# Optimization experiments

Hardware: AMD Instinct MI355X
Metric: run time of the kernel (lower is better)

The kernel has to match this reference:

```python
import jax, jax.numpy as jnp
import numpy as np

B, C, D = 8192, 10000, 128
CLAMP_MIN, CLAMP_MAX = 1e-12, 1e12


def setup_inputs() -> dict:
    key = jax.random.key(0)
    k1, k2, k3 = jax.random.split(key, 3)
    x = jax.random.normal(k1, (B, D), dtype=jnp.float32)
    labels = jax.random.randint(k2, (B,), 0, C, dtype=jnp.int64)
    centers = jax.random.normal(k3, (C, D), dtype=jnp.float32)
    lr = jnp.array([0.1], dtype=jnp.float32)
    return {"x": x, "labels": labels, "centers": centers, "lr": lr}


def reference(x, labels, centers, lr):
    b, d = x.shape
    c = centers.shape[0]
    # --- vectorized center update (replaces double python loop) ---
    # A_j = count_j * centers[j] - sum_{i: labels_i==j} x_i ; delta_j = A_j / (1 + count_j)
    counts = jax.ops.segment_sum(jnp.ones((b,), dtype=x.dtype), labels, num_segments=c)  # [C]
    sum_x = jax.ops.segment_sum(x, labels, num_segments=c)                               # [C, D]
    delta = (counts[:, None] * centers - sum_x) / (1.0 + counts[:, None])
    centers = centers - lr * delta
    # --- squared euclidean distance matrix [B, C] ---
    distmat = (
        jnp.sum(x * x, axis=1, keepdims=True)
        + jnp.sum(centers * centers, axis=1)[None, :]
        - 2.0 * (x @ centers.T)
    )
    git = 1.0 / (1.0 + distmat)
    # gather own-class entries (replaces per-sample mask loop)
    lab = labels[:, None]
    center_vals = jnp.take_along_axis(distmat, lab, axis=1)[:, 0]          # [B]
    git_vals = jnp.sum(git, axis=1) - jnp.take_along_axis(git, lab, axis=1)[:, 0]
    center_loss = jnp.mean(jnp.clip(center_vals, CLAMP_MIN, CLAMP_MAX))
    git_loss = jnp.mean(jnp.clip(git_vals, CLAMP_MIN, CLAMP_MAX))
    return (center_loss, git_loss)
```

## Files before the change

### kernel.cpp

```cpp
#include <hip/hip_runtime.h>
#include <hip/hip_bf16.h>
#include <hip/hip_fp8.h>

#define B_ 8192
#define C_ 10000
#define D_ 128
#define CPAD 10112
#define NPADC 112
#define NT_TOT 158
#define NSTRIP 16
#define STRIPW 10
#define UPD_BLOCKS 2528
#define CVAL_BLOCKS 2048

typedef float f32x4 __attribute__((ext_vector_type(4)));
typedef int   i32x8 __attribute__((ext_vector_type(8)));

typedef const __attribute__((address_space(1))) uint32_t gu32;
typedef __attribute__((address_space(3))) uint32_t lu32;


__global__ void zero_ws(float4* __restrict__ ws, float* __restrict__ out) {
    int idx = blockIdx.x * 256 + threadIdx.x;
    if (idx < 324608) ws[idx] = float4{0.f, 0.f, 0.f, 0.f};
    if (idx == 0) { out[0] = 0.f; out[1] = 0.f; }
}

__global__ void scatter_prep(const float* __restrict__ x, const int* __restrict__ labels,
                             float* __restrict__ counts, float* __restrict__ sumx,
                             float* __restrict__ xnorm, unsigned char* __restrict__ xb8) {
    int tid = threadIdx.x;
    int w = tid >> 6, lane = tid & 63;
    int i = blockIdx.x * 4 + w;
    int l = labels[i];
    float2 v = *(const float2*)&x[i * D_ + lane * 2];
    atomicAdd(&sumx[l * D_ + lane * 2], v.x);
    atomicAdd(&sumx[l * D_ + lane * 2 + 1], v.y);
    if (lane == 0) atomicAdd(&counts[l], 1.0f);
    __hip_fp8_e4m3 a(v.x), b(v.y);
    unsigned short pk = (unsigned short)a.__x | ((unsigned short)b.__x << 8);
    *(unsigned short*)&xb8[i * D_ + lane * 2] = pk;
    float s = v.x * v.x + v.y * v.y;
    #pragma unroll
    for (int m = 1; m < 64; m <<= 1) s += __shfl_xor(s, m);
    if (lane == 0) xnorm[i] = s;
}

__global__ void upd_cvals(const float* __restrict__ centers, const float* __restrict__ counts,
                          const float* __restrict__ sumx, float* __restrict__ cnorm,
                          unsigned char* __restrict__ cb8, const float* __restrict__ lr,
                          const float* __restrict__ x, const int* __restrict__ labels,
                          float* __restrict__ cent_val) {
    int tid = threadIdx.x;
    int w = tid >> 6, lane = tid & 63;
    int bid = blockIdx.x;
    float lrv = lr[0];

    if (bid < UPD_BLOCKS) {
        int c = bid * 4 + w;
        if (c >= C_) {
            *(unsigned short*)&cb8[c * D_ + lane * 2] = 0;
            if (lane == 0) cnorm[c] = 0.0f;
            return;
        }
        float cnt = counts[c];
        float2 cv = *(const float2*)&centers[c * D_ + lane * 2];
        float2 sx = *(const float2*)&sumx[c * D_ + lane * 2];
        float inv = 1.0f / (1.0f + cnt);
        float nx = cv.x - lrv * (cnt * cv.x - sx.x) * inv;
        float ny = cv.y - lrv * (cnt * cv.y - sx.y) * inv;
        __hip_fp8_e4m3 a(nx), b(ny);
        unsigned short pk = (unsigned short)a.__x | ((unsigned short)b.__x << 8);
        *(unsigned short*)&cb8[c * D_ + lane * 2] = pk;
        float s = nx * nx + ny * ny;
        #pragma unroll
        for (int m = 1; m < 64; m <<= 1) s += __shfl_xor(s, m);
        if (lane == 0) cnorm[c] = s;
    } else {
        int i = (bid - UPD_BLOCKS) * 4 + w;
        int l = labels[i];
        float cnt = counts[l];
        float inv = 1.0f / (1.0f + cnt);
        float2 a  = *(const float2*)&x[i * D_ + lane * 2];
        float2 cv = *(const float2*)&centers[l * D_ + lane * 2];
        float2 sx = *(const float2*)&sumx[l * D_ + lane * 2];
        float nx = cv.x - lrv * (cnt * cv.x - sx.x) * inv;
        float ny = cv.y - lrv * (cnt * cv.y - sx.y) * inv;
        float dx = a.x - nx, dy = a.y - ny;
        float s = dx * dx + dy * dy;
        #pragma unroll
        for (int m = 1; m < 64; m <<= 1) s += __shfl_xor(s, m);
        if (lane == 0) cent_val[i] = s;
    }
}

__global__ void __launch_bounds__(256, 2)
gemm_git(const unsigned char* __restrict__ xb8, const unsigned char* __restrict__ cb8,
         const float* __restrict__ xnorm, const float* __restrict__ cnorm,
         float* __restrict__ git_row) {
    __shared__ char ldsB[3][8192];
    __shared__ float cnLDS[STRIPW * 64];

    int tid = threadIdx.x;
    int w = tid >> 6, lane = tid & 63;
    int lr_ = lane & 15, lg = lane >> 4;
    int bm = blockIdx.x;
    int strip = blockIdx.y;
    int row0 = bm * 256 + w * 64;
    int bn0 = strip * STRIPW;
    int nt = (strip == NSTRIP - 1) ? (NT_TOT - bn0) : STRIPW;

    i32x8 af[4];
    #pragma unroll
    for (int f = 0; f < 4; f++) {
        const uint4* pa = (const uint4*)(xb8 + (size_t)(row0 + f * 16 + lr_) * 128 + lg * 32);
        uint4 u0 = pa[0], u1 = pa[1];
        asm volatile("" : "+v"(u0.x), "+v"(u0.y), "+v"(u0.z), "+v"(u0.w),
                          "+v"(u1.x), "+v"(u1.y), "+v"(u1.z), "+v"(u1.w));
        af[f] = i32x8{(int)u0.x, (int)u0.y, (int)u0.z, (int)u0.w,
                      (int)u1.x, (int)u1.y, (int)u1.z, (int)u1.w};
    }

    float xn1[4][4];
    #pragma unroll
    for (int fm = 0; fm < 4; fm++)
        #pragma unroll
        for (int r = 0; r < 4; r++) {
            float v = 1.0f + xnorm[row0 + fm * 16 + lg * 4 + r];
            asm volatile("" : "+v"(v));
            xn1[fm][r] = v;
        }

    float gitsum[4][4] = {};

    const char* gB = (const char*)cb8;
    int sr0 = tid >> 3,          sc0 = (tid & 7) ^ (sr0 & 7);
    int sr1 = (tid + 256) >> 3,  sc1 = ((tid + 256) & 7) ^ (sr1 & 7);
    size_t goff0 = (size_t)sr0 * 128 + sc0 * 16;
    size_t goff1 = (size_t)sr1 * 128 + sc1 * 16;

    auto stage = [&](int t, int buf) {
        const char* base = gB + (size_t)(bn0 + t) * 64 * 128;
        __builtin_amdgcn_global_load_lds((gu32*)(base + goff0),
                                         (lu32*)&ldsB[buf][tid * 16], 16, 0, 0);
        __builtin_amdgcn_global_load_lds((gu32*)(base + goff1),
                                         (lu32*)&ldsB[buf][4096 + tid * 16], 16, 0, 0);
    };

    for (int i = tid; i < nt * 64; i += 256) cnLDS[i] = cnorm[bn0 * 64 + i];
    stage(0, 0);
    if (nt > 1) stage(1, 1);
    __syncthreads();

    for (int t = 0; t < nt; ++t) {
        int bc = t % 3;
        if (t + 2 < nt) stage(t + 2, (t + 2) % 3);

        if (t + 2 < nt)      asm volatile("s_waitcnt vmcnt(4)" ::: "memory");
        else if (t + 1 < nt) asm volatile("s_waitcnt vmcnt(2)" ::: "memory");
        else                 asm volatile("s_waitcnt vmcnt(0)" ::: "memory");
        __builtin_amdgcn_sched_barrier(0);
        __builtin_amdgcn_s_barrier();
        __builtin_amdgcn_sched_barrier(0);

        float cn[4];
        #pragma unroll
        for (int fn = 0; fn < 4; fn++) cn[fn] = cnLDS[t * 64 + fn * 16 + lr_];

        i32x8 bfk[4];
        int r7 = lr_ & 7;
        #pragma unroll
        for (int fn = 0; fn < 4; fn++) {
            const char* rowp = &ldsB[bc][(fn * 16 + lr_) * 128];
            uint4 q0 = *(const uint4*)(rowp + (((lg * 2)     ^ r7) * 16));
            uint4 q1 = *(const uint4*)(rowp + (((lg * 2 + 1) ^ r7) * 16));
            bfk[fn] = i32x8{(int)q0.x, (int)q0.y, (int)q0.z, (int)q0.w,
                            (int)q1.x, (int)q1.y, (int)q1.z, (int)q1.w};
        }

        f32x4 acc[4][4] = {};
        __builtin_amdgcn_s_setprio(1);
        #pragma unroll
        for (int fm = 0; fm < 4; fm++)
            #pragma unroll
            for (int fn = 0; fn < 4; fn++)
                acc[fm][fn] = __builtin_amdgcn_mfma_scale_f32_16x16x128_f8f6f4(
                    af[fm], bfk[fn], acc[fm][fn],
                    0, 0,
                    0, 0x7F,
                    0, 0x7F);
        __builtin_amdgcn_s_setprio(0);

        #pragma unroll
        for (int fm = 0; fm < 4; fm++)
            #pragma unroll
            for (int r = 0; r < 4; r++) {
                float base = xn1[fm][r];
                #pragma unroll
                for (int fp = 0; fp < 4; fp += 2) {
                    float u = base + cn[fp]     - 2.0f * acc[fm][fp][r];
                    float v = base + cn[fp + 1] - 2.0f * acc[fm][fp + 1][r];
                    gitsum[fm][r] += (u + v) * __builtin_amdgcn_rcpf(u * v);
                }
            }

        __builtin_amdgcn_sched_barrier(0);
        __builtin_amdgcn_s_barrier();
        __builtin_amdgcn_sched_barrier(0);
    }

    #pragma unroll
    for (int fm = 0; fm < 4; fm++)
        #pragma unroll
        for (int r = 0; r < 4; r++) {
            float s = gitsum[fm][r];
            s += __shfl_xor(s, 1); s += __shfl_xor(s, 2);
            s += __shfl_xor(s, 4); s += __shfl_xor(s, 8);
            if (lr_ == 0) atomicAdd(&git_row[row0 + fm * 16 + lg * 4 + r], s);
        }
}

__global__ void final_reduce(const float* __restrict__ cent_val, const float* __restrict__ git_row,
                             const float* __restrict__ xnorm, float* __restrict__ out) {
    int tid = threadIdx.x;
    int i = blockIdx.x * 256 + tid;
    float c = cent_val[i];
    float cl = fminf(fmaxf(c, 1e-12f), 1e12f);
    float g = git_row[i] - 1.0f / (1.0f + c) - (float)NPADC / (1.0f + xnorm[i]);
    float gl = fminf(fmaxf(g, 1e-12f), 1e12f);
    #pragma unroll
    for (int m = 1; m < 64; m <<= 1) { cl += __shfl_xor(cl, m); gl += __shfl_xor(gl, m); }
    __shared__ float scl[4], sgl[4];
    if ((tid & 63) == 0) { scl[tid >> 6] = cl; sgl[tid >> 6] = gl; }
    __syncthreads();
    if (tid == 0) {
        float a = scl[0] + scl[1] + scl[2] + scl[3];
        float b = sgl[0] + sgl[1] + sgl[2] + sgl[3];
        atomicAdd(&out[0], a / (float)B_);
        atomicAdd(&out[1], b / (float)B_);
    }
}

extern "C" void kernel_launch(void* const* d_in, const int* in_sizes, int n_in,
                              void* d_out, int out_size, void* d_ws, size_t ws_size,
                              hipStream_t stream) {
    const float* x       = (const float*)d_in[0];
    const int*   labels  = (const int*)d_in[1];
    const float* centers = (const float*)d_in[2];
    const float* lr      = (const float*)d_in[3];

    float* ws       = (float*)d_ws;
    float* counts   = ws;
    float* sumx     = ws + 10240;
    float* git_row  = ws + 1290240;
    float* xnorm    = ws + 1298432;
    float* cent_val = ws + 1306624;
    float* cnorm    = ws + 1314816;
    unsigned char* xb8 = (unsigned char*)d_ws + 5300224;
    unsigned char* cb8 = (unsigned char*)d_ws + 7397376;
    float* out = (float*)d_out;

    zero_ws<<<1268, 256, 0, stream>>>((float4*)d_ws, out);
    scatter_prep<<<B_ / 4, 256, 0, stream>>>(x, labels, counts, sumx, xnorm, xb8);
    upd_cvals<<<UPD_BLOCKS + CVAL_BLOCKS, 256, 0, stream>>>(centers, counts, sumx, cnorm, cb8, lr,
                                                            x, labels, cent_val);
    gemm_git<<<dim3(32, NSTRIP), 256, 0, stream>>>(xb8, cb8, xnorm, cnorm, git_row);
    final_reduce<<<32, 256, 0, stream>>>(cent_val, git_row, xnorm, out);
}
```

Before: 50.29 us.

## Stage two center tiles per pipeline step and drop the trailing barrier

Each LDS stage of the FP8 GEMM now holds two 64-column center tiles instead of one, so the triple-buffered loop runs half as many iterations. The prefetch of stage s+2 is issued right after the per-iteration barrier, into the buffer freed by iteration s-1. That lets the end-of-iteration barrier go, leaving one barrier per two tiles instead of two per tile. The cost is double the LDS per block (48KB) and a longer gap between each wait and its consumer, which could limit occupancy or exposed latency.

```diff
diff --git a/kernel.cpp b/kernel.cpp
--- a/kernel.cpp
+++ b/kernel.cpp
@@ -98,7 +98,7 @@
 gemm_git(const unsigned char* __restrict__ xb8, const unsigned char* __restrict__ cb8,
          const float* __restrict__ xnorm, const float* __restrict__ cnorm,
          float* __restrict__ git_row) {
-    __shared__ char ldsB[3][8192];
+    __shared__ char ldsB[3][16384];
     __shared__ float cnLDS[STRIPW * 64];
 
     int tid = threadIdx.x;
@@ -109,6 +109,7 @@
     int row0 = bm * 256 + w * 64;
     int bn0 = strip * STRIPW;
     int nt = (strip == NSTRIP - 1) ? (NT_TOT - bn0) : STRIPW;
+    int ns = nt >> 1;
 
     i32x8 af[4];
     #pragma unroll
@@ -134,79 +135,82 @@
     float gitsum[4][4] = {};
 
     const char* gB = (const char*)cb8;
-    int sr0 = tid >> 3,          sc0 = (tid & 7) ^ (sr0 & 7);
-    int sr1 = (tid + 256) >> 3,  sc1 = ((tid + 256) & 7) ^ (sr1 & 7);
-    size_t goff0 = (size_t)sr0 * 128 + sc0 * 16;
-    size_t goff1 = (size_t)sr1 * 128 + sc1 * 16;
-
-    auto stage = [&](int t, int buf) {
-        const char* base = gB + (size_t)(bn0 + t) * 64 * 128;
-        __builtin_amdgcn_global_load_lds((gu32*)(base + goff0),
-                                         (lu32*)&ldsB[buf][tid * 16], 16, 0, 0);
-        __builtin_amdgcn_global_load_lds((gu32*)(base + goff1),
-                                         (lu32*)&ldsB[buf][4096 + tid * 16], 16, 0, 0);
+    size_t goff[4];
+    #pragma unroll
+    for (int p = 0; p < 4; p++) {
+        int idx = tid + p * 256;
+        int sr = idx >> 3, sc = (idx & 7) ^ (sr & 7);
+        goff[p] = (size_t)sr * 128 + sc * 16;
+    }
+
+    auto stage = [&](int s, int buf) {
+        const char* base = gB + (size_t)(bn0 + 2 * s) * 64 * 128;
+        #pragma unroll
+        for (int p = 0; p < 4; p++)
+            __builtin_amdgcn_global_load_lds((gu32*)(base + goff[p]),
+                                             (lu32*)&ldsB[buf][(tid + p * 256) * 16], 16, 0, 0);
     };
 
     for (int i = tid; i < nt * 64; i += 256) cnLDS[i] = cnorm[bn0 * 64 + i];
     stage(0, 0);
-    if (nt > 1) stage(1, 1);
+    if (ns > 1) stage(1, 1);
     __syncthreads();
 
-    for (int t = 0; t < nt; ++t) {
-        int bc = t % 3;
-        if (t + 2 < nt) stage(t + 2, (t + 2) % 3);
-
-        if (t + 2 < nt)      asm volatile("s_waitcnt vmcnt(4)" ::: "memory");
-        else if (t + 1 < nt) asm volatile("s_waitcnt vmcnt(2)" ::: "memory");
-        else                 asm volatile("s_waitcnt vmcnt(0)" ::: "memory");
+    for (int s = 0; s < ns; ++s) {
+        int bc = s % 3;
+
+        if (s + 1 < ns) asm volatile("s_waitcnt vmcnt(4)" ::: "memory");
+        else            asm volatile("s_waitcnt vmcnt(0)" ::: "memory");
         __builtin_amdgcn_sched_barrier(0);
         __builtin_amdgcn_s_barrier();
         __builtin_amdgcn_sched_barrier(0);
 
-        float cn[4];
-        #pragma unroll
-        for (int fn = 0; fn < 4; fn++) cn[fn] = cnLDS[t * 64 + fn * 16 + lr_];
-
-        i32x8 bfk[4];
-        int r7 = lr_ & 7;
-        #pragma unroll
-        for (int fn = 0; fn < 4; fn++) {
-            const char* rowp = &ldsB[bc][(fn * 16 + lr_) * 128];
-            uint4 q0 = *(const uint4*)(rowp + (((lg * 2)     ^ r7) * 16));
-            uint4 q1 = *(const uint4*)(rowp + (((lg * 2 + 1) ^ r7) * 16));
-            bfk[fn] = i32x8{(int)q0.x, (int)q0.y, (int)q0.z, (int)q0.w,
-                            (int)q1.x, (int)q1.y, (int)q1.z, (int)q1.w};
-        }
-
-        f32x4 acc[4][4] = {};
-        __builtin_amdgcn_s_setprio(1);
-        #pragma unroll
-        for (int fm = 0; fm < 4; fm++)
-            #pragma unroll
-            for (int fn = 0; fn < 4; fn++)
-                acc[fm][fn] = __builtin_amdgcn_mfma_scale_f32_16x16x128_f8f6f4(
-                    af[fm], bfk[fn], acc[fm][fn],
-                    0, 0,
-                    0, 0x7F,
-                    0, 0x7F);
-        __builtin_amdgcn_s_setprio(0);
-
-        #pragma unroll
-        for (int fm = 0; fm < 4; fm++)
-            #pragma unroll
-            for (int r = 0; r < 4; r++) {
-                float base = xn1[fm][r];
+        if (s + 2 < ns) stage(s + 2, (s + 2) % 3);
+
+        #pragma unroll
+        for (int h = 0; h < 2; ++h) {
+            int t = 2 * s + h;
+            float cn[4];
+            #pragma unroll
+            for (int fn = 0; fn < 4; fn++) cn[fn] = cnLDS[t * 64 + fn * 16 + lr_];
+
+            i32x8 bfk[4];
+            int r7 = lr_ & 7;
+            #pragma unroll
+            for (int fn = 0; fn < 4; fn++) {
+                const char* rowp = &ldsB[bc][(h * 64 + fn * 16 + lr_) * 128];
+                uint4 q0 = *(const uint4*)(rowp + (((lg * 2)     ^ r7) * 16));
+                uint4 q1 = *(const uint4*)(rowp + (((lg * 2 + 1) ^ r7) * 16));
+                bfk[fn] = i32x8{(int)q0.x, (int)q0.y, (int)q0.z, (int)q0.w,
+                                (int)q1.x, (int)q1.y, (int)q1.z, (int)q1.w};
+            }
+
+            f32x4 acc[4][4] = {};
+            __builtin_amdgcn_s_setprio(1);
+            #pragma unroll
+            for (int fm = 0; fm < 4; fm++)
                 #pragma unroll
-                for (int fp = 0; fp < 4; fp += 2) {
-                    float u = base + cn[fp]     - 2.0f * acc[fm][fp][r];
-                    float v = base + cn[fp + 1] - 2.0f * acc[fm][fp + 1][r];
-                    gitsum[fm][r] += (u + v) * __builtin_amdgcn_rcpf(u * v);
+                for (int fn = 0; fn < 4; fn++)
+                    acc[fm][fn] = __builtin_amdgcn_mfma_scale_f32_16x16x128_f8f6f4(
+                        af[fm], bfk[fn], acc[fm][fn],
+                        0, 0,
+                        0, 0x7F,
+                        0, 0x7F);
+            __builtin_amdgcn_s_setprio(0);
+
+            #pragma unroll
+            for (int fm = 0; fm < 4; fm++)
+                #pragma unroll
+                for (int r = 0; r < 4; r++) {
+                    float base = xn1[fm][r];
+                    #pragma unroll
+                    for (int fp = 0; fp < 4; fp += 2) {
+                        float u = base + cn[fp]     - 2.0f * acc[fm][fp][r];
+                        float v = base + cn[fp + 1] - 2.0f * acc[fm][fp + 1][r];
+                        gitsum[fm][r] += (u + v) * __builtin_amdgcn_rcpf(u * v);
+                    }
                 }
-            }
-
-        __builtin_amdgcn_sched_barrier(0);
-        __builtin_amdgcn_s_barrier();
-        __builtin_amdgcn_sched_barrier(0);
+        }
     }
 
     #pragma unroll
```

After: 60.91 us. 21.1% more time.
